# Kernel tuning notes

Hardware: AMD Instinct MI355X
Metric: run time of the kernel (lower is better)

The kernel has to match this reference:

```python
import jax, jax.numpy as jnp
import numpy as np

EPS_N = 1e-12   # F.normalize eps
LN_EPS = 1e-5   # LayerNorm eps
N_NODES = 20000
NODES_PER_GRAPH = 200
DEG = 8
N_EDGES = N_NODES * DEG
F_NODE = 36
F_EDGE = 10
HID = 128
HEAD = 8
DK = HID // HEAD
G = N_NODES // NODES_PER_GRAPH


def l2norm(x):
    n = jnp.sqrt(jnp.sum(x * x, axis=-1, keepdims=True))
    return x / jnp.maximum(n, EPS_N)


def layer_norm(x, g, b):
    m = jnp.mean(x, axis=-1, keepdims=True)
    v = jnp.mean((x - m) ** 2, axis=-1, keepdims=True)
    return (x - m) / jnp.sqrt(v + LN_EPS) * g + b


def seg_softmax(e, idx, n):
    m = jax.ops.segment_max(e, idx, num_segments=n)
    ex = jnp.exp(e - m[idx])
    s = jax.ops.segment_sum(ex, idx, num_segments=n)
    return ex / s[idx]


def sfe_conv(x, src, dst, eattr, We, Wq, Wk, Wv, Wo, bo, g, b):
    # x: [N, in], src/dst: [Ef] (self loops included), eattr: [Ef, F_EDGE]
    n = x.shape[0]
    emb = l2norm(eattr @ We)                  # edge_encoder + F.normalize
    xj = x[src] + emb                          # source node + edge embedding
    q = (xj @ Wq).reshape(-1, HEAD, DK)
    ksum = (x[dst] @ Wk).reshape(-1, HEAD, DK).sum(axis=1)  # sum over k-heads (matmul+sum in source)
    v = (xj @ Wv).reshape(-1, HEAD, DK)
    energy = jnp.einsum('ehd,ed->eh', q, ksum) / jnp.sqrt(jnp.float32(HID))
    att = seg_softmax(energy, dst, n)          # segment softmax over target nodes, per head
    msg = (v * att[:, :, None]).reshape(-1, HID)
    agg = jax.ops.segment_sum(msg, dst, num_segments=n)
    y = layer_norm(agg @ Wo + bo, g, b)        # update(): out_norm(out_linear(.))
    return layer_norm(y, g, b)                 # forward() applies out_norm again


def setup_inputs():
    key = jax.random.key(0)
    ks = jax.random.split(key, 16)
    x = jax.random.normal(ks[0], (N_NODES, F_NODE), jnp.float32)
    edge_attr = jax.random.uniform(ks[1], (N_EDGES, F_EDGE), jnp.float32)
    src = jnp.repeat(jnp.arange(N_NODES), DEG)
    base = src - src % NODES_PER_GRAPH
    off = jax.random.randint(ks[2], (N_EDGES,), 1, NODES_PER_GRAPH)
    dst = base + (src % NODES_PER_GRAPH + off) % NODES_PER_GRAPH  # same-graph, no self loops
    edge_index = jnp.stack([src, dst]).astype(jnp.int64)
    batch = (jnp.arange(N_NODES) // NODES_PER_GRAPH).astype(jnp.int64)
    interface_pos = jnp.arange(0, N_NODES, 2, dtype=jnp.int64)
    s = lambda k, sh: jax.random.normal(k, sh, jnp.float32) * 0.05
    return dict(
        x=x, edge_attr=edge_attr,
        c0_We=s(ks[3], (F_EDGE, F_NODE)), c0_Wq=s(ks[4], (F_NODE, HID)),
        c0_Wk=s(ks[5], (F_NODE, HID)), c0_Wv=s(ks[6], (F_NODE, HID)),
        c0_Wo=s(ks[7], (HID, HID)), c0_bo=jnp.zeros((HID,), jnp.float32),
        c0_g=jnp.ones((HID,), jnp.float32), c0_b=jnp.zeros((HID,), jnp.float32),
        cs_We=s(ks[8], (2, F_EDGE, HID)), cs_Wq=s(ks[9], (2, HID, HID)),
        cs_Wk=s(ks[10], (2, HID, HID)), cs_Wv=s(ks[11], (2, HID, HID)),
        cs_Wo=s(ks[12], (2, HID, HID)), cs_bo=jnp.zeros((2, HID), jnp.float32),
        cs_g=jnp.ones((2, HID), jnp.float32), cs_b=jnp.zeros((2, HID), jnp.float32),
        gate=s(ks[13], (HID,)), W1=s(ks[14], (HID, HID // 2)),
        b1=jnp.zeros((HID // 2,), jnp.float32), W2=s(ks[15], (HID // 2, 1)),
        b2=jnp.zeros((1,), jnp.float32),
        edge_index=edge_index, batch=batch, interface_pos=interface_pos,
        graph_num=G)


def reference(x, edge_attr, c0_We, c0_Wq, c0_Wk, c0_Wv, c0_Wo, c0_bo, c0_g, c0_b,
              cs_We, cs_Wq, cs_Wk, cs_Wv, cs_Wo, cs_bo, cs_g, cs_b,
              gate, W1, b1, W2, b2, edge_index, batch, interface_pos, graph_num):
    n = x.shape[0]
    loops = jnp.arange(n)
    src = jnp.concatenate([edge_index[0], loops])
    dst = jnp.concatenate([edge_index[1], loops])
    ea = jnp.concatenate([l2norm(edge_attr),
                          jnp.zeros((n, edge_attr.shape[1]), edge_attr.dtype)])
    h = l2norm(x)
    h = jnp.tanh(sfe_conv(h, src, dst, ea, c0_We, c0_Wq, c0_Wk, c0_Wv, c0_Wo, c0_bo, c0_g, c0_b))
    for i in range(cs_We.shape[0]):
        h = jnp.tanh(sfe_conv(h, src, dst, ea, cs_We[i], cs_Wq[i], cs_Wk[i], cs_Wv[i],
                              cs_Wo[i], cs_bo[i], cs_g[i], cs_b[i]))
    # global self-attention pooling over interface nodes, per graph
    xi = h[interface_pos]
    bi = batch[interface_pos]
    att = seg_softmax(xi @ gate, bi, graph_num)
    pooled = jax.ops.segment_sum(att[:, None] * xi, bi, num_segments=graph_num)  # [G, HID]
    out = jnp.tanh(pooled @ W1 + b1)
    return jax.nn.sigmoid(out @ W2 + b2)  # [G, 1]
```

## Files before the change

### kernel.cpp

```cpp
#include <hip/hip_runtime.h>
#include <math.h>

#define HID 128
#define HEAD 8
#define DK 16
#define FEDGE 10
#define FNODE 36
#define ESCALE 0.08838834764831845f
#define CH 32

typedef float f32x4v __attribute__((ext_vector_type(4)));
typedef short bf16x8 __attribute__((ext_vector_type(8)));

struct PackArgs {
  const float* src[8];
  unsigned short* dst[8];
  int fin[8];
  int kt[8];
  int blk_off[8];
};

struct PrepArgs {
  const float* We[3];
  const float* Wq[3];
  const float* Wk[3];
  const float* Wv[3];
  float* C[3];
  float* WeWv[3];
  float* Gram[3];
  float* Wksum[3];
  int fin[3];
};

__device__ __forceinline__ void fma4(float4& z, float s, const float4& w) {
  z.x += s * w.x;
  z.y += s * w.y;
  z.z += s * w.z;
  z.w += s * w.w;
}

__device__ __forceinline__ unsigned short f2bf(float f) {
  unsigned int u = __float_as_uint(f);
  u += 0x7fffu + ((u >> 16) & 1u);
  return (unsigned short)(u >> 16);
}

__device__ __forceinline__ float bflo(unsigned int u) { return __uint_as_float(u << 16); }
__device__ __forceinline__ float bfhi(unsigned int u) { return __uint_as_float(u & 0xffff0000u); }

__device__ __forceinline__ void store_bf8(unsigned short* p, float4 a, float4 b) {
  uint4 u;
  u.x = (unsigned)f2bf(a.x) | ((unsigned)f2bf(a.y) << 16);
  u.y = (unsigned)f2bf(a.z) | ((unsigned)f2bf(a.w) << 16);
  u.z = (unsigned)f2bf(b.x) | ((unsigned)f2bf(b.y) << 16);
  u.w = (unsigned)f2bf(b.z) | ((unsigned)f2bf(b.w) << 16);
  *(uint4*)p = u;
}

__global__ void k_zero_i(int* __restrict__ p, int n) {
  int i = blockIdx.x * 256 + threadIdx.x;
  if (i < n) p[i] = 0;
}

__global__ void k_count(const int* __restrict__ ei, int E, int* __restrict__ cnt) {
  int e = blockIdx.x * 256 + threadIdx.x;
  if (e >= E) return;
  atomicAdd(&cnt[ei[E + e]], 1);
}

__global__ __launch_bounds__(1024) void k_scan(const int* __restrict__ cnt, int* __restrict__ off,
                                               int* __restrict__ cur, int* __restrict__ scsr_s,
                                               int n, int total) {
  __shared__ int s[1024];
  int t = threadIdx.x;
  const int C = (n + 1023) / 1024;
  int local[32];
  int base = t * C;
  int sum = 0;
  for (int j = 0; j < C; ++j) {
    int i = base + j;
    int v = (i < n) ? cnt[i] : 0;
    local[j] = sum;
    sum += v;
  }
  s[t] = sum;
  __syncthreads();
  for (int dd = 1; dd < 1024; dd <<= 1) {
    int v = (t >= dd) ? s[t - dd] : 0;
    __syncthreads();
    s[t] += v;
    __syncthreads();
  }
  int excl = (t == 0) ? 0 : s[t - 1];
  for (int j = 0; j < C; ++j) {
    int i = base + j;
    if (i < n) {
      int o = excl + local[j];
      off[i] = o;
      cur[i] = o;
      scsr_s[o + i] = i;
    }
  }
  if (t == 0) off[n] = total;
}

__global__ void k_fill_sea(const int* __restrict__ ei, int E, int* __restrict__ cur,
                           int* __restrict__ scsr_s, const float* __restrict__ eattr,
                           const float* __restrict__ Gram3, float* __restrict__ sea3, int ET) {
  int e = blockIdx.x * 256 + threadIdx.x;
  if (e >= E) return;
  int t = ei[E + e];
  int pos = atomicAdd(&cur[t], 1) + t + 1;
  scsr_s[pos] = ei[e];
  float a[FEDGE];
  float ss = 0.f;
  for (int i = 0; i < FEDGE; ++i) {
    a[i] = eattr[(size_t)e * FEDGE + i];
    ss += a[i] * a[i];
  }
  float s0 = 1.f / fmaxf(sqrtf(ss), 1e-12f);
  for (int i = 0; i < FEDGE; ++i) a[i] *= s0;
  for (int l = 0; l < 3; ++l) {
    const float* G = Gram3 + l * FEDGE * FEDGE;
    float gp = 0.f;
#pragma unroll
    for (int j = 0; j < FEDGE; ++j) {
      float tt = 0.f;
#pragma unroll
      for (int u = 0; u < FEDGE; ++u) tt += G[j * FEDGE + u] * a[u];
      gp += tt * a[j];
    }
    float scl = 1.f / fmaxf(sqrtf(gp), 1e-12f);
    float* sp = sea3 + (size_t)l * ET * FEDGE + (size_t)pos * FEDGE;
#pragma unroll
    for (int u = 0; u < FEDGE; ++u) sp[u] = scl * a[u];
  }
}

__global__ __launch_bounds__(128) void k_wprep3(PrepArgs a) {
  int l = blockIdx.x / FEDGE, t = blockIdx.x - l * FEDGE;
  int d = threadIdx.x;
  int fin = a.fin[l];
  const float* We = a.We[l];
  const float* Wq = a.Wq[l];
  const float* Wk = a.Wk[l];
  const float* Wv = a.Wv[l];
  __shared__ float sw[HID];
  if (d < fin) sw[d] = We[t * fin + d];
  __syncthreads();
  float c = 0.f, wv = 0.f;
  for (int i = 0; i < fin; ++i) {
    c += sw[i] * Wq[i * HID + d];
    wv += sw[i] * Wv[i * HID + d];
  }
  a.C[l][t * HID + d] = c;
  a.WeWv[l][t * HID + d] = wv;
  if (d < FEDGE) {
    float g = 0.f;
    for (int i = 0; i < fin; ++i) g += sw[i] * We[d * fin + i];
    a.Gram[l][t * FEDGE + d] = g;
  }
  for (int r = t; r < fin; r += FEDGE) {
    if (d < DK) {
      float s = 0.f;
#pragma unroll
      for (int hh = 0; hh < HEAD; ++hh) s += Wk[r * HID + hh * DK + d];
      a.Wksum[l][r * DK + d] = s;
    }
  }
}

__global__ __launch_bounds__(64) void k_wpack8(PackArgs pa) {
  int b = blockIdx.x, lane = threadIdx.x;
  int m = 0;
#pragma unroll
  for (int i = 1; i < 8; ++i) m += (b >= pa.blk_off[i]);
  int local = b - pa.blk_off[m];
  int KT = pa.kt[m];
  int ct = local / KT, kt = local - ct * KT;
  const float* W = pa.src[m];
  int fin = pa.fin[m];
  int col = ct * 16 + (lane & 15);
  int kbase = kt * 32 + (lane >> 4) * 8;
  float v[8];
#pragma unroll
  for (int j = 0; j < 8; ++j) {
    int k = kbase + j;
    v[j] = (k < fin) ? W[k * HID + col] : 0.f;
  }
  store_bf8(pa.dst[m] + (size_t)local * 512 + lane * 8, make_float4(v[0], v[1], v[2], v[3]),
            make_float4(v[4], v[5], v[6], v[7]));
}

__global__ __launch_bounds__(256) void k1_l2x(
    const float* __restrict__ x, const unsigned short* __restrict__ qpack,
    const unsigned short* __restrict__ vpack, const float* __restrict__ Wksum,
    const float* __restrict__ C, unsigned short* __restrict__ qxh, float* __restrict__ kb,
    unsigned short* __restrict__ vxh, float* __restrict__ Mout, int N) {
  const int fin = FNODE;
  int d = threadIdx.x;
  int n0 = blockIdx.x * 16;
  int nb = min(16, N - n0);
  __shared__ __align__(16) float sx[16][40];
  __shared__ __align__(16) unsigned short afrag[2][64][8];
  __shared__ float sk[16][DK];
  {
    int col = d & 127, h2 = d >> 7;
#pragma unroll
    for (int rr = 0; rr < 8; ++rr) {
      int r = h2 * 8 + rr;
      if (col < fin) sx[r][col] = (r < nb) ? x[(size_t)(n0 + r) * fin + col] : 0.f;
    }
  }
  __syncthreads();
  int grp = d >> 4, j16 = d & 15;
  {
    float ssq = 0.f;
    for (int i = j16; i < fin; i += 16) ssq += sx[grp][i] * sx[grp][i];
#pragma unroll
    for (int o = 8; o; o >>= 1) ssq += __shfl_xor(ssq, o, 16);
    float scl = 1.f / fmaxf(sqrtf(ssq), 1e-12f);
    for (int i = j16; i < fin; i += 16) sx[grp][i] *= scl;
  }
  __syncthreads();
  int lane = d & 63, wvid = d >> 6;
  if (d < 128) {
    int kt = d >> 6;
    int m = lane & 15, k0 = kt * 32 + (lane >> 4) * 8;
    float v[8];
#pragma unroll
    for (int j = 0; j < 8; ++j) {
      int k = k0 + j;
      v[j] = (k < fin) ? sx[m][k] : 0.f;
    }
    store_bf8(&afrag[kt][lane][0], make_float4(v[0], v[1], v[2], v[3]),
              make_float4(v[4], v[5], v[6], v[7]));
  }
  {
    float kk = 0.f;
    for (int i = 0; i < fin; ++i) kk += sx[grp][i] * Wksum[i * DK + j16];
    sk[grp][j16] = kk;
    if (grp < nb) kb[(size_t)(n0 + grp) * DK + j16] = kk;
  }
  __syncthreads();
  int colD = lane & 15, quad = lane >> 4;
#pragma unroll
  for (int t = 0; t < 4; ++t) {
    int g = wvid * 4 + t;
    int mat = g >> 3, ct = g & 7;
    const unsigned short* P = mat ? vpack : qpack;
    f32x4v acc = {0.f, 0.f, 0.f, 0.f};
#pragma unroll
    for (int kt = 0; kt < 2; ++kt) {
      bf16x8 a = *(const bf16x8*)&afrag[kt][lane][0];
      bf16x8 b = *(const bf16x8*)(P + ((size_t)(ct * 2 + kt) * 64 + lane) * 8);
      acc = __builtin_amdgcn_mfma_f32_16x16x32_bf16(a, b, acc, 0, 0, 0);
    }
    unsigned short* out = mat ? vxh : qxh;
#pragma unroll
    for (int reg = 0; reg < 4; ++reg) {
      int node = quad * 4 + reg;
      if (node < nb) out[(size_t)(n0 + node) * HID + ct * 16 + colD] = f2bf(acc[reg]);
    }
  }
  if (d < HEAD * FEDGE) {
    int hh = d / FEDGE, tt = d - hh * FEDGE;
    float crow[16];
    *(float4*)&crow[0] = *(const float4*)&C[tt * HID + hh * DK + 0];
    *(float4*)&crow[4] = *(const float4*)&C[tt * HID + hh * DK + 4];
    *(float4*)&crow[8] = *(const float4*)&C[tt * HID + hh * DK + 8];
    *(float4*)&crow[12] = *(const float4*)&C[tt * HID + hh * DK + 12];
    for (int r = 0; r < nb; ++r) {
      float m = 0.f;
#pragma unroll
      for (int j = 0; j < DK; ++j) m += sk[r][j] * crow[j];
      Mout[((size_t)(n0 + r) * HEAD + hh) * 16 + tt] = m;
    }
  }
}

__global__ __launch_bounds__(256) void k_post_k1(
    const float* __restrict__ agg, const unsigned short* __restrict__ opack,
    const float* __restrict__ bo, const float* __restrict__ gg, const float* __restrict__ bb,
    const unsigned short* __restrict__ qpack, const unsigned short* __restrict__ vpack,
    const float* __restrict__ Wksum, const float* __restrict__ C,
    unsigned short* __restrict__ qxh, float* __restrict__ kb, unsigned short* __restrict__ vxh,
    float* __restrict__ Mout, int N) {
  int d = threadIdx.x;
  int n0 = blockIdx.x * 16;
  int nb = min(16, N - n0);
  __shared__ __align__(16) unsigned short afrag[4][64][8];
  __shared__ __align__(16) float sz[16][132];
  __shared__ __align__(16) unsigned short hfrag[4][64][8];
  __shared__ float sk[16][DK];
  int lane = d & 63, wvid = d >> 6;
  {
    int kt = wvid;
    int m = lane & 15, k0 = kt * 32 + (lane >> 4) * 8;
    const float* p = agg + (size_t)(n0 + m) * HID + k0;
    float4 x0 = *(const float4*)p;
    float4 x1 = *(const float4*)(p + 4);
    store_bf8(&afrag[kt][lane][0], x0, x1);
  }
  __syncthreads();
  int colD = lane & 15, quad = lane >> 4;
  {
    int ct0 = wvid * 2, ct1 = wvid * 2 + 1;
    float bias0 = bo[ct0 * 16 + colD], bias1 = bo[ct1 * 16 + colD];
    f32x4v acc0 = {bias0, bias0, bias0, bias0};
    f32x4v acc1 = {bias1, bias1, bias1, bias1};
#pragma unroll
    for (int kt = 0; kt < 4; ++kt) {
      bf16x8 a = *(const bf16x8*)&afrag[kt][lane][0];
      bf16x8 b0 = *(const bf16x8*)(opack + ((size_t)(ct0 * 4 + kt) * 64 + lane) * 8);
      bf16x8 b1 = *(const bf16x8*)(opack + ((size_t)(ct1 * 4 + kt) * 64 + lane) * 8);
      acc0 = __builtin_amdgcn_mfma_f32_16x16x32_bf16(a, b0, acc0, 0, 0, 0);
      acc1 = __builtin_amdgcn_mfma_f32_16x16x32_bf16(a, b1, acc1, 0, 0, 0);
    }
#pragma unroll
    for (int reg = 0; reg < 4; ++reg) {
      int node = quad * 4 + reg;
      sz[node][ct0 * 16 + colD] = acc0[reg];
      sz[node][ct1 * 16 + colD] = acc1[reg];
    }
  }
  __syncthreads();
  {
    int c4 = d & 31, rs = d >> 5;
    int col0 = c4 * 4, r0 = rs * 2;
    float4 zA = *(const float4*)&sz[r0][col0];
    float4 zB = *(const float4*)&sz[r0 + 1][col0];
    float4 g4 = *(const float4*)&gg[col0];
    float4 b4 = *(const float4*)&bb[col0];
#pragma unroll
    for (int pass = 0; pass < 2; ++pass) {
      float sA = zA.x + zA.y + zA.z + zA.w;
      float qA = zA.x * zA.x + zA.y * zA.y + zA.z * zA.z + zA.w * zA.w;
      float sB = zB.x + zB.y + zB.z + zB.w;
      float qB = zB.x * zB.x + zB.y * zB.y + zB.z * zB.z + zB.w * zB.w;
#pragma unroll
      for (int o = 16; o; o >>= 1) {
        sA += __shfl_xor(sA, o, 32);
        qA += __shfl_xor(qA, o, 32);
        sB += __shfl_xor(sB, o, 32);
        qB += __shfl_xor(qB, o, 32);
      }
      float mA = sA * (1.f / 128.f);
      float iA = rsqrtf(fmaxf(qA * (1.f / 128.f) - mA * mA, 0.f) + 1e-5f);
      float mB = sB * (1.f / 128.f);
      float iB = rsqrtf(fmaxf(qB * (1.f / 128.f) - mB * mB, 0.f) + 1e-5f);
      zA.x = (zA.x - mA) * iA * g4.x + b4.x;
      zA.y = (zA.y - mA) * iA * g4.y + b4.y;
      zA.z = (zA.z - mA) * iA * g4.z + b4.z;
      zA.w = (zA.w - mA) * iA * g4.w + b4.w;
      zB.x = (zB.x - mB) * iB * g4.x + b4.x;
      zB.y = (zB.y - mB) * iB * g4.y + b4.y;
      zB.z = (zB.z - mB) * iB * g4.z + b4.z;
      zB.w = (zB.w - mB) * iB * g4.w + b4.w;
    }
    zA.x = tanhf(zA.x);
    zA.y = tanhf(zA.y);
    zA.z = tanhf(zA.z);
    zA.w = tanhf(zA.w);
    zB.x = tanhf(zB.x);
    zB.y = tanhf(zB.y);
    zB.z = tanhf(zB.z);
    zB.w = tanhf(zB.w);
    *(float4*)&sz[r0][col0] = zA;
    *(float4*)&sz[r0 + 1][col0] = zB;
    int chunk = col0 >> 5, qd = (col0 >> 3) & 3, eo = col0 & 7;
    unsigned int loA = (unsigned)f2bf(zA.x) | ((unsigned)f2bf(zA.y) << 16);
    unsigned int hiA = (unsigned)f2bf(zA.z) | ((unsigned)f2bf(zA.w) << 16);
    unsigned int loB = (unsigned)f2bf(zB.x) | ((unsigned)f2bf(zB.y) << 16);
    unsigned int hiB = (unsigned)f2bf(zB.z) | ((unsigned)f2bf(zB.w) << 16);
    unsigned short* pA = &hfrag[chunk][(r0 & 15) + qd * 16][eo];
    unsigned short* pB = &hfrag[chunk][((r0 + 1) & 15) + qd * 16][eo];
    *(unsigned int*)pA = loA;
    *(unsigned int*)(pA + 2) = hiA;
    *(unsigned int*)pB = loB;
    *(unsigned int*)(pB + 2) = hiB;
  }
  __syncthreads();
#pragma unroll
  for (int t = 0; t < 4; ++t) {
    int g = wvid * 4 + t;
    int mat = g >> 3, ct = g & 7;
    const unsigned short* P = mat ? vpack : qpack;
    f32x4v acc = {0.f, 0.f, 0.f, 0.f};
#pragma unroll
    for (int kt = 0; kt < 4; ++kt) {
      bf16x8 a = *(const bf16x8*)&hfrag[kt][lane][0];
      bf16x8 b = *(const bf16x8*)(P + ((size_t)(ct * 4 + kt) * 64 + lane) * 8);
      acc = __builtin_amdgcn_mfma_f32_16x16x32_bf16(a, b, acc, 0, 0, 0);
    }
    unsigned short* out = mat ? vxh : qxh;
#pragma unroll
    for (int reg = 0; reg < 4; ++reg) {
      int node = quad * 4 + reg;
      if (node < nb) out[(size_t)(n0 + node) * HID + ct * 16 + colD] = f2bf(acc[reg]);
    }
  }
  int grp = d >> 4, j16 = d & 15;
  {
    float kk = 0.f;
    for (int i = 0; i < HID; ++i) kk += sz[grp][i] * Wksum[i * DK + j16];
    sk[grp][j16] = kk;
    if (grp < nb) kb[(size_t)(n0 + grp) * DK + j16] = kk;
  }
  __syncthreads();
  if (d < HEAD * FEDGE) {
    int hh = d / FEDGE, tt = d - hh * FEDGE;
    float crow[16];
    *(float4*)&crow[0] = *(const float4*)&C[tt * HID + hh * DK + 0];
    *(float4*)&crow[4] = *(const float4*)&C[tt * HID + hh * DK + 4];
    *(float4*)&crow[8] = *(const float4*)&C[tt * HID + hh * DK + 8];
    *(float4*)&crow[12] = *(const float4*)&C[tt * HID + hh * DK + 12];
    for (int r = 0; r < nb; ++r) {
      float m = 0.f;
#pragma unroll
      for (int j = 0; j < DK; ++j) m += sk[r][j] * crow[j];
      Mout[((size_t)(n0 + r) * HEAD + hh) * 16 + tt] = m;
    }
  }
}

__global__ __launch_bounds__(128) void k3_gather(
    const int* __restrict__ off, const int* __restrict__ scsr_s, const float* __restrict__ sea,
    const unsigned short* __restrict__ qxh, const float* __restrict__ kb,
    const float* __restrict__ Mbuf, const unsigned short* __restrict__ vxh,
    const float* __restrict__ WeWv, float* __restrict__ agg, int N,
    const int* __restrict__ nodemap, int use_map) {
  int b = blockIdx.x;
  int n, oi;
  if (use_map) {
    n = nodemap[b];
    oi = b;
  } else {
    n = ((N & 7) == 0) ? ((b & 7) * (N >> 3) + (b >> 3)) : b;
    oi = n;
  }
  int d = threadIdx.x;
  int j16 = d & 15, hd = d >> 4;
  __shared__ float sen[CH * 8];
  __shared__ float ssea[CH * 10];
  __shared__ int ss[CH];
  __shared__ float sT[HEAD * FEDGE];
  __shared__ __align__(16) float skb[DK];
  __shared__ float sM[128];
  int base = off[n] + n;
  int cnt = off[n + 1] + n + 1 - base;
  if (d < DK) skb[d] = kb[(size_t)n * DK + d];
  sM[d] = Mbuf[(size_t)n * 128 + d];
  bool doT = (j16 < FEDGE);
  float m = -1e30f, l = 0.f, accv = 0.f, T = 0.f;
  for (int c0 = 0; c0 < cnt; c0 += CH) {
    int cc = min(CH, cnt - c0);
    for (int idx = d; idx < cc * 10; idx += 128)
      ssea[idx] = sea[(size_t)(base + c0) * 10 + idx];
    if (d < cc) ss[d] = scsr_s[base + c0 + d];
    __syncthreads();
    for (int ob = 0; ob < cc; ob += 16) {
      int o = ob + (d >> 3);
      int h = d & 7;
      if (o < cc) {
        int s = ss[o];
        const uint4* qp = (const uint4*)(qxh + (size_t)s * HID + h * DK);
        uint4 qa = qp[0], qb = qp[1];
        float en = bflo(qa.x) * skb[0] + bfhi(qa.x) * skb[1] + bflo(qa.y) * skb[2] +
                   bfhi(qa.y) * skb[3] + bflo(qa.z) * skb[4] + bfhi(qa.z) * skb[5] +
                   bflo(qa.w) * skb[6] + bfhi(qa.w) * skb[7] + bflo(qb.x) * skb[8] +
                   bfhi(qb.x) * skb[9] + bflo(qb.y) * skb[10] + bfhi(qb.y) * skb[11] +
                   bflo(qb.z) * skb[12] + bfhi(qb.z) * skb[13] + bflo(qb.w) * skb[14] +
                   bfhi(qb.w) * skb[15];
        if ((c0 + o) > 0) {
#pragma unroll
          for (int u = 0; u < FEDGE; ++u) en += sM[h * DK + u] * ssea[o * 10 + u];
        }
        sen[o * 8 + h] = en * ESCALE;
      }
    }
    __syncthreads();
    float mloc = -1e30f;
    for (int o = 0; o < cc; ++o) mloc = fmaxf(mloc, sen[o * 8 + hd]);
    float mnew = fmaxf(m, mloc);
    float alpha = __expf(m - mnew);
    l *= alpha;
    accv *= alpha;
    T *= alpha;
#pragma unroll 2
    for (int o = 0; o < cc; ++o) {
      int s = ss[o];
      float p = __expf(sen[o * 8 + hd] - mnew);
      l += p;
      float vv = __uint_as_float((unsigned)vxh[(size_t)s * HID + d] << 16);
      accv += p * vv;
      if (doT && (c0 + o) > 0) T += p * ssea[o * 10 + j16];
    }
    m = mnew;
    __syncthreads();
  }
  float inv = 1.f / l;
  if (doT) sT[hd * FEDGE + j16] = T * inv;
  __syncthreads();
  float y = accv * inv;
#pragma unroll
  for (int t = 0; t < FEDGE; ++t) y += sT[hd * FEDGE + t] * WeWv[t * HID + d];
  agg[(size_t)oi * HID + d] = y;
}

__global__ __launch_bounds__(256) void k_post(const float* __restrict__ agg,
                                              const float* __restrict__ Wo,
                                              const float* __restrict__ bo,
                                              const float* __restrict__ gg,
                                              const float* __restrict__ bb,
                                              float* __restrict__ hout, int N) {
  int d = threadIdx.x;
  int n0 = blockIdx.x * 16;
  int nb = min(16, N - n0);
  __shared__ __align__(16) float sh[16][132];
  {
    int col = d & 127, h2 = d >> 7;
#pragma unroll
    for (int rr = 0; rr < 8; ++rr) {
      int r = h2 * 8 + rr;
      sh[r][col] = (r < nb) ? agg[(size_t)(n0 + r) * HID + col] : 0.f;
    }
  }
  __syncthreads();
  int c4 = d & 31, rs = d >> 5;
  int col0 = c4 * 4, r0 = rs * 2;
  float4 bv = *(const float4*)&bo[col0];
  float4 zA = bv, zB = bv;
  for (int k4 = 0; k4 < 32; ++k4) {
    float4 w0 = *(const float4*)&Wo[(k4 * 4 + 0) * HID + col0];
    float4 w1 = *(const float4*)&Wo[(k4 * 4 + 1) * HID + col0];
    float4 w2 = *(const float4*)&Wo[(k4 * 4 + 2) * HID + col0];
    float4 w3 = *(const float4*)&Wo[(k4 * 4 + 3) * HID + col0];
    float4 a0 = *(const float4*)&sh[r0][k4 * 4];
    float4 a1 = *(const float4*)&sh[r0 + 1][k4 * 4];
    fma4(zA, a0.x, w0);
    fma4(zA, a0.y, w1);
    fma4(zA, a0.z, w2);
    fma4(zA, a0.w, w3);
    fma4(zB, a1.x, w0);
    fma4(zB, a1.y, w1);
    fma4(zB, a1.z, w2);
    fma4(zB, a1.w, w3);
  }
  float4 g4 = *(const float4*)&gg[col0];
  float4 b4 = *(const float4*)&bb[col0];
#pragma unroll
  for (int pass = 0; pass < 2; ++pass) {
    float sA = zA.x + zA.y + zA.z + zA.w;
    float qA = zA.x * zA.x + zA.y * zA.y + zA.z * zA.z + zA.w * zA.w;
    float sB = zB.x + zB.y + zB.z + zB.w;
    float qB = zB.x * zB.x + zB.y * zB.y + zB.z * zB.z + zB.w * zB.w;
#pragma unroll
    for (int o = 16; o; o >>= 1) {
      sA += __shfl_xor(sA, o, 32);
      qA += __shfl_xor(qA, o, 32);
      sB += __shfl_xor(sB, o, 32);
      qB += __shfl_xor(qB, o, 32);
    }
    float mA = sA * (1.f / 128.f);
    float iA = rsqrtf(fmaxf(qA * (1.f / 128.f) - mA * mA, 0.f) + 1e-5f);
    float mB = sB * (1.f / 128.f);
    float iB = rsqrtf(fmaxf(qB * (1.f / 128.f) - mB * mB, 0.f) + 1e-5f);
    zA.x = (zA.x - mA) * iA * g4.x + b4.x;
    zA.y = (zA.y - mA) * iA * g4.y + b4.y;
    zA.z = (zA.z - mA) * iA * g4.z + b4.z;
    zA.w = (zA.w - mA) * iA * g4.w + b4.w;
    zB.x = (zB.x - mB) * iB * g4.x + b4.x;
    zB.y = (zB.y - mB) * iB * g4.y + b4.y;
    zB.z = (zB.z - mB) * iB * g4.z + b4.z;
    zB.w = (zB.w - mB) * iB * g4.w + b4.w;
  }
  if (r0 < nb) {
    float4 o0 = make_float4(tanhf(zA.x), tanhf(zA.y), tanhf(zA.z), tanhf(zA.w));
    *(float4*)&hout[(size_t)(n0 + r0) * HID + col0] = o0;
  }
  if (r0 + 1 < nb) {
    float4 o1 = make_float4(tanhf(zB.x), tanhf(zB.y), tanhf(zB.z), tanhf(zB.w));
    *(float4*)&hout[(size_t)(n0 + r0 + 1) * HID + col0] = o1;
  }
}

__global__ __launch_bounds__(128) void k4_pool(const float* __restrict__ h,
                                               const float* __restrict__ gate,
                                               const float* __restrict__ W1,
                                               const float* __restrict__ b1,
                                               const float* __restrict__ W2,
                                               const float* __restrict__ b2,
                                               float* __restrict__ out, int per_g) {
  int g = blockIdx.x, d = threadIdx.x;
  __shared__ float satt[128], spool[HID], so[64], sv[2];
  size_t rbase = (size_t)g * per_g;
  float sc = -1e30f;
  if (d < per_g) {
    float s = 0.f;
    const float* hp = h + (rbase + d) * HID;
    for (int i = 0; i < HID; ++i) s += hp[i] * gate[i];
    sc = s;
  }
  satt[d] = sc;
  __syncthreads();
  if (d == 0) {
    float m = -1e30f;
    for (int i = 0; i < per_g; ++i) m = fmaxf(m, satt[i]);
    sv[0] = m;
  }
  __syncthreads();
  float m = sv[0];
  float ex = (d < per_g) ? __expf(sc - m) : 0.f;
  satt[d] = ex;
  __syncthreads();
  if (d == 0) {
    float su = 0.f;
    for (int i = 0; i < per_g; ++i) su += satt[i];
    sv[1] = 1.f / su;
  }
  __syncthreads();
  float inv = sv[1];
  float p = 0.f;
  for (int i = 0; i < per_g; ++i) p += satt[i] * h[(rbase + i) * HID + d];
  spool[d] = p * inv;
  __syncthreads();
  if (d < 64) {
    float o = b1[d];
    for (int i = 0; i < HID; ++i) o += spool[i] * W1[i * 64 + d];
    so[d] = tanhf(o);
  }
  __syncthreads();
  if (d == 0) {
    float z = b2[0];
    for (int i = 0; i < 64; ++i) z += so[i] * W2[i];
    out[g] = 1.f / (1.f + __expf(-z));
  }
}

extern "C" void kernel_launch(void* const* d_in, const int* in_sizes, int n_in, void* d_out,
                              int out_size, void* d_ws, size_t ws_size, hipStream_t stream) {
  const float* x = (const float*)d_in[0];
  const float* eattr = (const float*)d_in[1];
  const float* c0_We = (const float*)d_in[2];
  const float* c0_Wq = (const float*)d_in[3];
  const float* c0_Wk = (const float*)d_in[4];
  const float* c0_Wv = (const float*)d_in[5];
  const float* c0_Wo = (const float*)d_in[6];
  const float* c0_bo = (const float*)d_in[7];
  const float* c0_g = (const float*)d_in[8];
  const float* c0_b = (const float*)d_in[9];
  const float* cs_We = (const float*)d_in[10];
  const float* cs_Wq = (const float*)d_in[11];
  const float* cs_Wk = (const float*)d_in[12];
  const float* cs_Wv = (const float*)d_in[13];
  const float* cs_Wo = (const float*)d_in[14];
  const float* cs_bo = (const float*)d_in[15];
  const float* cs_g = (const float*)d_in[16];
  const float* cs_b = (const float*)d_in[17];
  const float* gate = (const float*)d_in[18];
  const float* W1 = (const float*)d_in[19];
  const float* b1 = (const float*)d_in[20];
  const float* W2 = (const float*)d_in[21];
  const float* b2 = (const float*)d_in[22];
  const int* ei = (const int*)d_in[23];
  const int* ipos = (const int*)d_in[25];

  int N = in_sizes[0] / FNODE;
  int E = in_sizes[1] / FEDGE;
  int G = out_size;
  int NI = in_sizes[25];
  int per_g = NI / G;
  int ET = E + N;

  float* w = (float*)d_ws;
  float* hB = w;         w += (size_t)N * HID;
  float* aggb = w;       w += (size_t)N * HID;
  float* kb = w;         w += (size_t)N * DK;
  float* Mbuf = w;       w += (size_t)N * HEAD * 16;
  float* sea3 = w;       w += (size_t)3 * ET * FEDGE;
  float* C3 = w;         w += 3 * FEDGE * HID;
  float* WeWv3 = w;      w += 3 * FEDGE * HID;
  float* Gram3 = w;      w += 3 * FEDGE * FEDGE;
  float* Wksum3 = w;     w += 3 * HID * DK;
  unsigned short* qxh = (unsigned short*)w;  w += (size_t)N * HID / 2;
  unsigned short* vxh = (unsigned short*)w;  w += (size_t)N * HID / 2;
  unsigned short* qp3 = (unsigned short*)w;  w += 3 * 16384 / 2;
  unsigned short* vp3 = (unsigned short*)w;  w += 3 * 16384 / 2;
  unsigned short* op2 = (unsigned short*)w;  w += 2 * 16384 / 2;
  int* cnt = (int*)w;
  int* off = cnt + (N + 1);
  int* cur = off + (N + 1);
  int* scsr_s = cur + N;

  const float* Ws[3][8] = {
      {c0_We, c0_Wq, c0_Wk, c0_Wv, c0_Wo, c0_bo, c0_g, c0_b},
      {cs_We, cs_Wq, cs_Wk, cs_Wv, cs_Wo, cs_bo, cs_g, cs_b},
      {cs_We + FEDGE * HID, cs_Wq + HID * HID, cs_Wk + HID * HID, cs_Wv + HID * HID,
       cs_Wo + HID * HID, cs_bo + HID, cs_g + HID, cs_b + HID}};
  int fins[3] = {FNODE, HID, HID};

  PrepArgs prep;
  for (int l = 0; l < 3; ++l) {
    prep.We[l] = Ws[l][0];
    prep.Wq[l] = Ws[l][1];
    prep.Wk[l] = Ws[l][2];
    prep.Wv[l] = Ws[l][3];
    prep.C[l] = C3 + l * FEDGE * HID;
    prep.WeWv[l] = WeWv3 + l * FEDGE * HID;
    prep.Gram[l] = Gram3 + l * FEDGE * FEDGE;
    prep.Wksum[l] = Wksum3 + l * HID * DK;
    prep.fin[l] = fins[l];
  }
  k_wprep3<<<3 * FEDGE, 128, 0, stream>>>(prep);

  PackArgs pa;
  {
    const float* srcs[8] = {Ws[0][1], Ws[0][3], Ws[1][1], Ws[1][3],
                            Ws[2][1], Ws[2][3], Ws[0][4], Ws[1][4]};
    unsigned short* dsts[8] = {qp3, vp3, qp3 + 16384, vp3 + 16384, qp3 + 2 * 16384,
                               vp3 + 2 * 16384, op2, op2 + 16384};
    int fns[8] = {FNODE, FNODE, HID, HID, HID, HID, HID, HID};
    int kts[8] = {2, 2, 4, 4, 4, 4, 4, 4};
    int offb = 0;
    for (int i = 0; i < 8; ++i) {
      pa.src[i] = srcs[i];
      pa.dst[i] = dsts[i];
      pa.fin[i] = fns[i];
      pa.kt[i] = kts[i];
      pa.blk_off[i] = offb;
      offb += 8 * kts[i];
    }
    k_wpack8<<<offb, 64, 0, stream>>>(pa);
  }

  k_zero_i<<<(N + 1 + 255) / 256, 256, 0, stream>>>(cnt, N + 1);
  k_count<<<(E + 255) / 256, 256, 0, stream>>>(ei, E, cnt);
  k_scan<<<1, 1024, 0, stream>>>(cnt, off, cur, scsr_s, N, E);
  k_fill_sea<<<(E + 255) / 256, 256, 0, stream>>>(ei, E, cur, scsr_s, eattr, Gram3, sea3, ET);

  k1_l2x<<<(N + 15) / 16, 256, 0, stream>>>(x, qp3, vp3, Wksum3, C3, qxh, kb, vxh, Mbuf, N);
  for (int l = 0; l < 3; ++l) {
    const float* sea_l = sea3 + (size_t)l * ET * FEDGE;
    if (l < 2) {
      k3_gather<<<N, 128, 0, stream>>>(off, scsr_s, sea_l, qxh, kb, Mbuf, vxh,
                                       WeWv3 + l * FEDGE * HID, aggb, N, ipos, 0);
      k_post_k1<<<(N + 15) / 16, 256, 0, stream>>>(
          aggb, op2 + l * 16384, Ws[l][5], Ws[l][6], Ws[l][7], qp3 + (l + 1) * 16384,
          vp3 + (l + 1) * 16384, Wksum3 + (l + 1) * HID * DK, C3 + (l + 1) * FEDGE * HID, qxh, kb,
          vxh, Mbuf, N);
    } else {
      k3_gather<<<NI, 128, 0, stream>>>(off, scsr_s, sea_l, qxh, kb, Mbuf, vxh,
                                        WeWv3 + l * FEDGE * HID, aggb, N, ipos, 1);
      k_post<<<(NI + 15) / 16, 256, 0, stream>>>(aggb, Ws[l][4], Ws[l][5], Ws[l][6], Ws[l][7], hB,
                                                 NI);
    }
  }
  k4_pool<<<G, 128, 0, stream>>>(hB, gate, W1, b1, W2, b2, (float*)d_out, per_g);
}
```

Measured before the change: 368.9 us.

## Merge setup kernels into one launch and process two nodes per gather block

Three small setup kernels (weight prep, weight packing, counter zeroing) are folded into a single launch that dispatches on block index, removing two kernel launches. The gather kernel now processes two destination nodes per 256-thread block, each half using its own shared-memory slots, which halves the block count and aims to improve occupancy and scheduling. Both halves loop to the larger of the two edge counts and share barriers, so the half with fewer edges sits idle for the extra iterations. For odd counts the last block computes the final node twice.

```diff
diff --git a/kernel.cpp b/kernel.cpp
--- a/kernel.cpp
+++ b/kernel.cpp
@@ -57,9 +57,69 @@
   *(uint4*)p = u;
 }
 
-__global__ void k_zero_i(int* __restrict__ p, int n) {
-  int i = blockIdx.x * 256 + threadIdx.x;
-  if (i < n) p[i] = 0;
+__global__ __launch_bounds__(256) void k_setup(PrepArgs a, PackArgs pa, int wprepN, int wpackN,
+                                               int* __restrict__ cnt, int nzero) {
+  int b = blockIdx.x, d = threadIdx.x;
+  __shared__ float sw[HID];
+  if (b < wprepN) {
+    int l = b / FEDGE, t = b - l * FEDGE;
+    int fin = a.fin[l];
+    const float* We = a.We[l];
+    if (d < fin) sw[d] = We[t * fin + d];
+    __syncthreads();
+    if (d < 128) {
+      const float* Wq = a.Wq[l];
+      const float* Wv = a.Wv[l];
+      const float* Wk = a.Wk[l];
+      float c = 0.f, wv = 0.f;
+      for (int i = 0; i < fin; ++i) {
+        c += sw[i] * Wq[i * HID + d];
+        wv += sw[i] * Wv[i * HID + d];
+      }
+      a.C[l][t * HID + d] = c;
+      a.WeWv[l][t * HID + d] = wv;
+      if (d < FEDGE) {
+        float g = 0.f;
+        for (int i = 0; i < fin; ++i) g += sw[i] * We[d * fin + i];
+        a.Gram[l][t * FEDGE + d] = g;
+      }
+      for (int r = t; r < fin; r += FEDGE) {
+        if (d < DK) {
+          float s = 0.f;
+#pragma unroll
+          for (int hh = 0; hh < HEAD; ++hh) s += Wk[r * HID + hh * DK + d];
+          a.Wksum[l][r * DK + d] = s;
+        }
+      }
+    }
+    return;
+  }
+  if (b < wprepN + wpackN) {
+    if (d >= 64) return;
+    int bb = b - wprepN;
+    int lane = d;
+    int m = 0;
+#pragma unroll
+    for (int i = 1; i < 8; ++i) m += (bb >= pa.blk_off[i]);
+    int local = bb - pa.blk_off[m];
+    int KT = pa.kt[m];
+    int ct = local / KT, kt = local - ct * KT;
+    const float* W = pa.src[m];
+    int fin = pa.fin[m];
+    int col = ct * 16 + (lane & 15);
+    int kbase = kt * 32 + (lane >> 4) * 8;
+    float v[8];
+#pragma unroll
+    for (int j = 0; j < 8; ++j) {
+      int k = kbase + j;
+      v[j] = (k < fin) ? W[k * HID + col] : 0.f;
+    }
+    store_bf8(pa.dst[m] + (size_t)local * 512 + lane * 8, make_float4(v[0], v[1], v[2], v[3]),
+              make_float4(v[4], v[5], v[6], v[7]));
+    return;
+  }
+  int i = (b - wprepN - wpackN) * 256 + d;
+  if (i < nzero) cnt[i] = 0;
 }
 
 __global__ void k_count(const int* __restrict__ ei, int E, int* __restrict__ cnt) {
@@ -135,61 +195,6 @@
 #pragma unroll
     for (int u = 0; u < FEDGE; ++u) sp[u] = scl * a[u];
   }
-}
-
-__global__ __launch_bounds__(128) void k_wprep3(PrepArgs a) {
-  int l = blockIdx.x / FEDGE, t = blockIdx.x - l * FEDGE;
-  int d = threadIdx.x;
-  int fin = a.fin[l];
-  const float* We = a.We[l];
-  const float* Wq = a.Wq[l];
-  const float* Wk = a.Wk[l];
-  const float* Wv = a.Wv[l];
-  __shared__ float sw[HID];
-  if (d < fin) sw[d] = We[t * fin + d];
-  __syncthreads();
-  float c = 0.f, wv = 0.f;
-  for (int i = 0; i < fin; ++i) {
-    c += sw[i] * Wq[i * HID + d];
-    wv += sw[i] * Wv[i * HID + d];
-  }
-  a.C[l][t * HID + d] = c;
-  a.WeWv[l][t * HID + d] = wv;
-  if (d < FEDGE) {
-    float g = 0.f;
-    for (int i = 0; i < fin; ++i) g += sw[i] * We[d * fin + i];
-    a.Gram[l][t * FEDGE + d] = g;
-  }
-  for (int r = t; r < fin; r += FEDGE) {
-    if (d < DK) {
-      float s = 0.f;
-#pragma unroll
-      for (int hh = 0; hh < HEAD; ++hh) s += Wk[r * HID + hh * DK + d];
-      a.Wksum[l][r * DK + d] = s;
-    }
-  }
-}
-
-__global__ __launch_bounds__(64) void k_wpack8(PackArgs pa) {
-  int b = blockIdx.x, lane = threadIdx.x;
-  int m = 0;
-#pragma unroll
-  for (int i = 1; i < 8; ++i) m += (b >= pa.blk_off[i]);
-  int local = b - pa.blk_off[m];
-  int KT = pa.kt[m];
-  int ct = local / KT, kt = local - ct * KT;
-  const float* W = pa.src[m];
-  int fin = pa.fin[m];
-  int col = ct * 16 + (lane & 15);
-  int kbase = kt * 32 + (lane >> 4) * 8;
-  float v[8];
-#pragma unroll
-  for (int j = 0; j < 8; ++j) {
-    int k = kbase + j;
-    v[j] = (k < fin) ? W[k * HID + col] : 0.f;
-  }
-  store_bf8(pa.dst[m] + (size_t)local * 512 + lane * 8, make_float4(v[0], v[1], v[2], v[3]),
-            make_float4(v[4], v[5], v[6], v[7]));
 }
 
 __global__ __launch_bounds__(256) void k1_l2x(
@@ -424,64 +429,68 @@
   }
 }
 
-__global__ __launch_bounds__(128) void k3_gather(
+__global__ __launch_bounds__(256) void k3_gather2(
     const int* __restrict__ off, const int* __restrict__ scsr_s, const float* __restrict__ sea,
     const unsigned short* __restrict__ qxh, const float* __restrict__ kb,
     const float* __restrict__ Mbuf, const unsigned short* __restrict__ vxh,
-    const float* __restrict__ WeWv, float* __restrict__ agg, int N,
+    const float* __restrict__ WeWv, float* __restrict__ agg, int count,
     const int* __restrict__ nodemap, int use_map) {
-  int b = blockIdx.x;
-  int n, oi;
-  if (use_map) {
-    n = nodemap[b];
-    oi = b;
-  } else {
-    n = ((N & 7) == 0) ? ((b & 7) * (N >> 3) + (b >> 3)) : b;
-    oi = n;
-  }
+  int pb = blockIdx.x;
   int d = threadIdx.x;
-  int j16 = d & 15, hd = d >> 4;
-  __shared__ float sen[CH * 8];
-  __shared__ float ssea[CH * 10];
-  __shared__ int ss[CH];
-  __shared__ float sT[HEAD * FEDGE];
-  __shared__ __align__(16) float skb[DK];
-  __shared__ float sM[128];
+  int half = d >> 7, d7 = d & 127;
+  int P = (count + 1) >> 1;
+  int p = ((P & 7) == 0) ? ((pb & 7) * (P >> 3) + (pb >> 3)) : pb;
+  int idx = 2 * p + half;
+  if (idx >= count) idx = count - 1;
+  int n = use_map ? nodemap[idx] : idx;
+  int oi = idx;
+  int j16 = d7 & 15, hd = d7 >> 4;
+  __shared__ float sen[2][CH * 8];
+  __shared__ float ssea[2][CH * 10];
+  __shared__ int ss[2][CH];
+  __shared__ float sT[2][HEAD * FEDGE];
+  __shared__ __align__(16) float skb[2][DK];
+  __shared__ float sM[2][128];
+  __shared__ int scnt[2];
   int base = off[n] + n;
   int cnt = off[n + 1] + n + 1 - base;
-  if (d < DK) skb[d] = kb[(size_t)n * DK + d];
-  sM[d] = Mbuf[(size_t)n * 128 + d];
+  if (d7 < DK) skb[half][d7] = kb[(size_t)n * DK + d7];
+  sM[half][d7] = Mbuf[(size_t)n * 128 + d7];
+  if (d7 == 0) scnt[half] = cnt;
+  __syncthreads();
+  int cmax = max(scnt[0], scnt[1]);
   bool doT = (j16 < FEDGE);
   float m = -1e30f, l = 0.f, accv = 0.f, T = 0.f;
-  for (int c0 = 0; c0 < cnt; c0 += CH) {
+  for (int c0 = 0; c0 < cmax; c0 += CH) {
     int cc = min(CH, cnt - c0);
-    for (int idx = d; idx < cc * 10; idx += 128)
-      ssea[idx] = sea[(size_t)(base + c0) * 10 + idx];
-    if (d < cc) ss[d] = scsr_s[base + c0 + d];
+    for (int idx2 = d7; idx2 < cc * 10; idx2 += 128)
+      ssea[half][idx2] = sea[(size_t)(base + c0) * 10 + idx2];
+    if (d7 < cc) ss[half][d7] = scsr_s[base + c0 + d7];
     __syncthreads();
     for (int ob = 0; ob < cc; ob += 16) {
-      int o = ob + (d >> 3);
-      int h = d & 7;
+      int o = ob + (d7 >> 3);
+      int h = d7 & 7;
       if (o < cc) {
-        int s = ss[o];
+        int s = ss[half][o];
         const uint4* qp = (const uint4*)(qxh + (size_t)s * HID + h * DK);
         uint4 qa = qp[0], qb = qp[1];
-        float en = bflo(qa.x) * skb[0] + bfhi(qa.x) * skb[1] + bflo(qa.y) * skb[2] +
-                   bfhi(qa.y) * skb[3] + bflo(qa.z) * skb[4] + bfhi(qa.z) * skb[5] +
-                   bflo(qa.w) * skb[6] + bfhi(qa.w) * skb[7] + bflo(qb.x) * skb[8] +
-                   bfhi(qb.x) * skb[9] + bflo(qb.y) * skb[10] + bfhi(qb.y) * skb[11] +
-                   bflo(qb.z) * skb[12] + bfhi(qb.z) * skb[13] + bflo(qb.w) * skb[14] +
-                   bfhi(qb.w) * skb[15];
+        const float* kbp = &skb[half][0];
+        float en = bflo(qa.x) * kbp[0] + bfhi(qa.x) * kbp[1] + bflo(qa.y) * kbp[2] +
+                   bfhi(qa.y) * kbp[3] + bflo(qa.z) * kbp[4] + bfhi(qa.z) * kbp[5] +
+                   bflo(qa.w) * kbp[6] + bfhi(qa.w) * kbp[7] + bflo(qb.x) * kbp[8] +
+                   bfhi(qb.x) * kbp[9] + bflo(qb.y) * kbp[10] + bfhi(qb.y) * kbp[11] +
+                   bflo(qb.z) * kbp[12] + bfhi(qb.z) * kbp[13] + bflo(qb.w) * kbp[14] +
+                   bfhi(qb.w) * kbp[15];
         if ((c0 + o) > 0) {
 #pragma unroll
-          for (int u = 0; u < FEDGE; ++u) en += sM[h * DK + u] * ssea[o * 10 + u];
+          for (int u = 0; u < FEDGE; ++u) en += sM[half][h * DK + u] * ssea[half][o * 10 + u];
         }
-        sen[o * 8 + h] = en * ESCALE;
+        sen[half][o * 8 + h] = en * ESCALE;
       }
     }
     __syncthreads();
     float mloc = -1e30f;
-    for (int o = 0; o < cc; ++o) mloc = fmaxf(mloc, sen[o * 8 + hd]);
+    for (int o = 0; o < cc; ++o) mloc = fmaxf(mloc, sen[half][o * 8 + hd]);
     float mnew = fmaxf(m, mloc);
     float alpha = __expf(m - mnew);
     l *= alpha;
@@ -489,23 +498,23 @@
     T *= alpha;
 #pragma unroll 2
     for (int o = 0; o < cc; ++o) {
-      int s = ss[o];
-      float p = __expf(sen[o * 8 + hd] - mnew);
-      l += p;
-      float vv = __uint_as_float((unsigned)vxh[(size_t)s * HID + d] << 16);
-      accv += p * vv;
-      if (doT && (c0 + o) > 0) T += p * ssea[o * 10 + j16];
+      int s = ss[half][o];
+      float pp = __expf(sen[half][o * 8 + hd] - mnew);
+      l += pp;
+      float vv = __uint_as_float((unsigned)vxh[(size_t)s * HID + d7] << 16);
+      accv += pp * vv;
+      if (doT && (c0 + o) > 0) T += pp * ssea[half][o * 10 + j16];
     }
     m = mnew;
     __syncthreads();
   }
   float inv = 1.f / l;
-  if (doT) sT[hd * FEDGE + j16] = T * inv;
+  if (doT) sT[half][hd * FEDGE + j16] = T * inv;
   __syncthreads();
   float y = accv * inv;
 #pragma unroll
-  for (int t = 0; t < FEDGE; ++t) y += sT[hd * FEDGE + t] * WeWv[t * HID + d];
-  agg[(size_t)oi * HID + d] = y;
+  for (int t = 0; t < FEDGE; ++t) y += sT[half][hd * FEDGE + t] * WeWv[t * HID + d7];
+  agg[(size_t)oi * HID + d7] = y;
 }
 
 __global__ __launch_bounds__(256) void k_post(const float* __restrict__ agg,
@@ -712,9 +721,8 @@
     prep.Wksum[l] = Wksum3 + l * HID * DK;
     prep.fin[l] = fins[l];
   }
-  k_wprep3<<<3 * FEDGE, 128, 0, stream>>>(prep);
-
   PackArgs pa;
+  int wpackN = 0;
   {
     const float* srcs[8] = {Ws[0][1], Ws[0][3], Ws[1][1], Ws[1][3],
                             Ws[2][1], Ws[2][3], Ws[0][4], Ws[1][4]};
@@ -722,19 +730,19 @@
                                vp3 + 2 * 16384, op2, op2 + 16384};
     int fns[8] = {FNODE, FNODE, HID, HID, HID, HID, HID, HID};
     int kts[8] = {2, 2, 4, 4, 4, 4, 4, 4};
-    int offb = 0;
     for (int i = 0; i < 8; ++i) {
       pa.src[i] = srcs[i];
       pa.dst[i] = dsts[i];
       pa.fin[i] = fns[i];
       pa.kt[i] = kts[i];
-      pa.blk_off[i] = offb;
-      offb += 8 * kts[i];
-    }
-    k_wpack8<<<offb, 64, 0, stream>>>(pa);
-  }
-
-  k_zero_i<<<(N + 1 + 255) / 256, 256, 0, stream>>>(cnt, N + 1);
+      pa.blk_off[i] = wpackN;
+      wpackN += 8 * kts[i];
+    }
+  }
+  int wprepN = 3 * FEDGE;
+  int zeroB = (N + 1 + 255) / 256;
+  k_setup<<<wprepN + wpackN + zeroB, 256, 0, stream>>>(prep, pa, wprepN, wpackN, cnt, N + 1);
+
   k_count<<<(E + 255) / 256, 256, 0, stream>>>(ei, E, cnt);
   k_scan<<<1, 1024, 0, stream>>>(cnt, off, cur, scsr_s, N, E);
   k_fill_sea<<<(E + 255) / 256, 256, 0, stream>>>(ei, E, cur, scsr_s, eattr, Gram3, sea3, ET);
@@ -743,15 +751,15 @@
   for (int l = 0; l < 3; ++l) {
     const float* sea_l = sea3 + (size_t)l * ET * FEDGE;
     if (l < 2) {
-      k3_gather<<<N, 128, 0, stream>>>(off, scsr_s, sea_l, qxh, kb, Mbuf, vxh,
-                                       WeWv3 + l * FEDGE * HID, aggb, N, ipos, 0);
+      k3_gather2<<<(N + 1) / 2, 256, 0, stream>>>(off, scsr_s, sea_l, qxh, kb, Mbuf, vxh,
+                                                  WeWv3 + l * FEDGE * HID, aggb, N, ipos, 0);
       k_post_k1<<<(N + 15) / 16, 256, 0, stream>>>(
           aggb, op2 + l * 16384, Ws[l][5], Ws[l][6], Ws[l][7], qp3 + (l + 1) * 16384,
           vp3 + (l + 1) * 16384, Wksum3 + (l + 1) * HID * DK, C3 + (l + 1) * FEDGE * HID, qxh, kb,
           vxh, Mbuf, N);
     } else {
-      k3_gather<<<NI, 128, 0, stream>>>(off, scsr_s, sea_l, qxh, kb, Mbuf, vxh,
-                                        WeWv3 + l * FEDGE * HID, aggb, N, ipos, 1);
+      k3_gather2<<<(NI + 1) / 2, 256, 0, stream>>>(off, scsr_s, sea_l, qxh, kb, Mbuf, vxh,
+                                                   WeWv3 + l * FEDGE * HID, aggb, NI, ipos, 1);
       k_post<<<(NI + 15) / 16, 256, 0, stream>>>(aggb, Ws[l][4], Ws[l][5], Ws[l][6], Ws[l][7], hB,
                                                  NI);
     }
```

Result: slower. 398.0 us (+7.9%).
